# Optimization experiments

Measured on AMD Instinct MI355X. Metric: run time of the kernel, lower is better.

## Reference

```python
import jax, jax.numpy as jnp
import numpy as np

B, S, D = 2, 2048, 256
N_LAYERS, H, DK, DV, DFF = 2, 8, 32, 32, 512
EPS2 = np.float32(np.finfo(np.float32).eps) ** 2  # module uses eps*eps


def setup_inputs() -> dict:
    key = jax.random.key(0)
    ks = jax.random.split(key, 8)
    def xav(k, shape, fi, fo):
        lim = np.sqrt(6.0 / (fi + fo)).astype(np.float32)
        return jax.random.uniform(k, shape, jnp.float32, -lim, lim)
    return {
        'x': jax.random.normal(ks[0], (B, S, D), jnp.float32),
        'Wq': xav(ks[1], (N_LAYERS, H, D, DK), D, DK),
        'Wk': xav(ks[2], (N_LAYERS, H, D, DK), D, DK),
        'Wv': xav(ks[3], (N_LAYERS, H, D, DV), D, DV),
        'Wo': xav(ks[4], (N_LAYERS, H * DV, D), H * DV, D),
        'W1': xav(ks[5], (N_LAYERS, D, DFF), D, DFF),
        'b1': jnp.zeros((N_LAYERS, DFF), jnp.float32),
        'W2': xav(ks[6], (N_LAYERS, DFF, D), DFF, D),
        'b2': jnp.zeros((N_LAYERS, D), jnp.float32),
        'gamma': jnp.ones((2 * N_LAYERS,), jnp.float32),
        'beta': jnp.zeros((2 * N_LAYERS,), jnp.float32),
    }


def _layernorm(x, g, b):
    m = jnp.mean(x, axis=-1, keepdims=True)
    v = jnp.mean((x - m) ** 2, axis=-1, keepdims=True)
    return (x - m) / jnp.sqrt(v + EPS2) * g + b


def reference(x, Wq, Wk, Wv, Wo, W1, b1, W2, b2, gamma, beta):
    # mask=None in the original -> all-ones mask, a mathematical no-op.
    # NOTE: no 1/sqrt(dk) scaling, matching the source.
    n_layers = Wq.shape[0]
    for i in range(n_layers):
        q = jnp.einsum('bsd,hdk->bhsk', x, Wq[i])
        k = jnp.einsum('bsd,hdk->bhsk', x, Wk[i])
        v = jnp.einsum('bsd,hdk->bhsk', x, Wv[i])
        A = jax.nn.softmax(jnp.einsum('bhqk,bhsk->bhqs', q, k), axis=-1)
        o = jnp.einsum('bhqs,bhsk->bhqk', A, v)  # [B,h,S,dv]
        b_, h_, s_, dv_ = o.shape
        conc = o.transpose(0, 2, 1, 3).reshape(b_, s_, h_ * dv_)  # concat heads in order
        x = x + conc @ Wo[i]
        x = _layernorm(x, gamma[2 * i], beta[2 * i])
        ffn = jax.nn.relu(x @ W1[i] + b1[i]) @ W2[i] + b2[i]
        x = _layernorm(x + ffn, gamma[2 * i + 1], beta[2 * i + 1])
    return x
```

## Files before the change

### kernel.cpp

```cpp
#include <hip/hip_runtime.h>
#include <math.h>

#define BB 2
#define SS 2048
#define DD 256
#define HH 8
#define DKK 32
#define DVV 32
#define DFF 512
#define NL 2

#define KT 64
#define KSTR 40
#define VSTR 72
#define PSTR 72
#define NSPLIT 4
#define SCHUNK (SS / NSPLIT)

#define XSTR 264
#define HSTR 520
#define YSTR 260

typedef __attribute__((ext_vector_type(8))) short short8;
typedef __attribute__((ext_vector_type(4))) float f32x4;

static __device__ __forceinline__ float ln_eps2() { return 1.4210854715202004e-14f; }

static __device__ __forceinline__ ushort f2bf(float f) {
    union { float f; unsigned u; } c; c.f = f;
    unsigned r = c.u + 0x7FFFu + ((c.u >> 16) & 1u);
    return (ushort)(r >> 16);
}
static __device__ __forceinline__ float bf2f(ushort h) {
    union { unsigned u; float f; } c; c.u = ((unsigned)h) << 16;
    return c.f;
}

__global__ __launch_bounds__(256) void wtrans_kernel(
    const float* __restrict__ W1, const float* __restrict__ W2,
    ushort* __restrict__ w1t_hi, ushort* __restrict__ w1t_lo,
    ushort* __restrict__ w2t_hi, ushort* __restrict__ w2t_lo)
{
    __shared__ ushort Th[64][72];
    __shared__ ushort Tl[64][72];
    const int bid = blockIdx.x;
    const float* src; ushort *dh, *dl; int R, C, tile;
    if (bid < 64) {
        const int l = bid >> 5; tile = bid & 31;
        src = W1 + (size_t)l * DD * DFF;
        dh = w1t_hi + (size_t)l * DFF * DD; dl = w1t_lo + (size_t)l * DFF * DD;
        R = DD; C = DFF;
    } else {
        const int l = (bid - 64) >> 5; tile = (bid - 64) & 31;
        src = W2 + (size_t)l * DFF * DD;
        dh = w2t_hi + (size_t)l * DD * DFF; dl = w2t_lo + (size_t)l * DD * DFF;
        R = DFF; C = DD;
    }
    const int tilesC = C / 64;
    const int br = (tile / tilesC) * 64, bc = (tile % tilesC) * 64;
    const int tid = threadIdx.x;
#pragma unroll
    for (int i = 0; i < 16; ++i) {
        const int p = i * 256 + tid;
        const int r = p >> 6, c = p & 63;
        const float f = src[(size_t)(br + r) * C + bc + c];
        const ushort h = f2bf(f);
        Th[c][r] = h; Tl[c][r] = f2bf(f - bf2f(h));
    }
    __syncthreads();
#pragma unroll
    for (int i = 0; i < 16; ++i) {
        const int p = i * 256 + tid;
        const int r = p >> 6, c = p & 63;
        dh[(size_t)(bc + r) * R + br + c] = Th[r][c];
        dl[(size_t)(bc + r) * R + br + c] = Tl[r][c];
    }
}

__global__ __launch_bounds__(256) void wotrans_kernel(
    const float* __restrict__ Wo,
    ushort* __restrict__ wh, ushort* __restrict__ wl)
{
    __shared__ float T[64][65];
    const int l = blockIdx.x >> 4, tile = blockIdx.x & 15;
    const int tr = (tile >> 2) * 64;
    const int tc = (tile & 3) * 64;
    const float* src = Wo + (size_t)l * DD * DD;
    ushort* dh = wh + (size_t)l * DD * DD;
    ushort* dl = wl + (size_t)l * DD * DD;
    const int tid = threadIdx.x;
#pragma unroll
    for (int i = 0; i < 16; ++i) {
        const int p = i * 256 + tid;
        const int r = p >> 6, c = p & 63;
        T[r][c] = src[(size_t)(tr + r) * DD + tc + c];
    }
    __syncthreads();
#pragma unroll
    for (int i = 0; i < 16; ++i) {
        const int p = i * 256 + tid;
        const int r = p >> 6, c = p & 63;
        const float f = T[c][r];
        const size_t off = (size_t)(tc + r) * DD + tr + c;
        const ushort h = f2bf(f);
        dh[off] = h;
        dl[off] = f2bf(f - bf2f(h));
    }
}

__global__ __launch_bounds__(256) void wqkv_trans_kernel(
    const float* __restrict__ Wq, const float* __restrict__ Wk,
    const float* __restrict__ Wv,
    ushort* __restrict__ qkvT_hi, ushort* __restrict__ qkvT_lo)
{
    __shared__ float T[DKK][DD + 1];
    const int bid = blockIdx.x;
    const int l = bid / 24, rem = bid % 24, src = rem >> 3, h = rem & 7;
    const float* W = (src == 0 ? Wq : src == 1 ? Wk : Wv)
                     + ((size_t)l * HH + h) * DD * DKK;
    ushort* dh = qkvT_hi + ((size_t)l * 768 + src * 256 + h * 32) * DD;
    ushort* dl = qkvT_lo + ((size_t)l * 768 + src * 256 + h * 32) * DD;
    const int tid = threadIdx.x;
#pragma unroll
    for (int i = 0; i < 32; ++i) {
        const int p = i * 256 + tid;
        T[p & 31][p >> 5] = W[p];
    }
    __syncthreads();
#pragma unroll
    for (int i = 0; i < 32; ++i) {
        const int p = i * 256 + tid;
        const int dk = p >> 8, d = p & 255;
        const float f = T[dk][d];
        const ushort hh = f2bf(f);
        dh[dk * DD + d] = hh;
        dl[dk * DD + d] = f2bf(f - bf2f(hh));
    }
}

__global__ __launch_bounds__(256) void qkv_mfma_kernel(
    const float* __restrict__ xin,
    const ushort* __restrict__ wth, const ushort* __restrict__ wtl,
    float* __restrict__ q, ushort* __restrict__ khi, ushort* __restrict__ klo,
    ushort* __restrict__ vt)
{
    __shared__ __align__(16) ushort Xh[16 * XSTR];
    __shared__ __align__(16) ushort Xl[16 * XSTR];

    const int tid = threadIdx.x, wave = tid >> 6, lane = tid & 63;
    const int c16 = lane & 15, g = lane >> 4;
    const int row0 = (blockIdx.x >> 1) * 16;
    const int half = blockIdx.x & 1;

#pragma unroll
    for (int i = 0; i < 16; ++i) {
        const int p = i * 256 + tid;
        const int r = p >> 8, c = p & 255;
        const float f = xin[(size_t)(row0 + r) * DD + c];
        const ushort h = f2bf(f);
        Xh[r * XSTR + c] = h;
        Xl[r * XSTR + c] = f2bf(f - bf2f(h));
    }
    __syncthreads();

    short8 xf_h[8], xf_l[8];
#pragma unroll
    for (int kk = 0; kk < 8; ++kk) {
        xf_h[kk] = *(const short8*)&Xh[c16 * XSTR + kk * 32 + g * 8];
        xf_l[kk] = *(const short8*)&Xl[c16 * XSTR + kk * 32 + g * 8];
    }

    const int b = row0 / SS, s0 = row0 % SS;
    const int wbase = half * 384 + wave * 96;
#pragma unroll 2
    for (int t = 0; t < 6; ++t) {
        const int ncol = wbase + t * 16 + c16;
        const ushort* wh = wth + (size_t)ncol * DD;
        const ushort* wl = wtl + (size_t)ncol * DD;
        f32x4 acc = (f32x4)(0.f);
#pragma unroll
        for (int kk = 0; kk < 8; ++kk) {
            const short8 bh = *(const short8*)(wh + kk * 32 + g * 8);
            const short8 bl = *(const short8*)(wl + kk * 32 + g * 8);
            acc = __builtin_amdgcn_mfma_f32_16x16x32_bf16(xf_h[kk], bh, acc, 0, 0, 0);
            acc = __builtin_amdgcn_mfma_f32_16x16x32_bf16(xf_l[kk], bh, acc, 0, 0, 0);
            acc = __builtin_amdgcn_mfma_f32_16x16x32_bf16(xf_h[kk], bl, acc, 0, 0, 0);
        }
        const int src = ncol >> 8, h = (ncol >> 5) & 7, dk = ncol & 31;
        const size_t base = ((size_t)(b * HH + h) * SS + s0) * DKK + dk;
#pragma unroll
        for (int r = 0; r < 4; ++r) {
            if (src == 0) {
                q[base + (size_t)(4 * g + r) * DKK] = acc[r];
            } else if (src == 1) {
                const size_t off = base + (size_t)(4 * g + r) * DKK;
                const ushort hh = f2bf(acc[r]);
                khi[off] = hh;
                klo[off] = f2bf(acc[r] - bf2f(hh));
            } else {
                vt[((size_t)(b * HH + h) * DVV + dk) * SS + s0 + 4 * g + r] = f2bf(acc[r]);
            }
        }
    }
}

__global__ __launch_bounds__(256) void attn_mfma_kernel(
    const float* __restrict__ q, const ushort* __restrict__ khi,
    const ushort* __restrict__ klo, const ushort* __restrict__ vt,
    float* __restrict__ opart, float* __restrict__ ml)
{
    __shared__ ushort KhS[KT * KSTR];
    __shared__ ushort KlS[KT * KSTR];
    __shared__ ushort VtS[32 * VSTR];
    __shared__ ushort PlS[4 * 16 * PSTR];

    const int tid  = threadIdx.x;
    const int wave = tid >> 6;
    const int lane = tid & 63;
    const int c16  = lane & 15;
    const int g    = lane >> 4;

    const int nqb = SS / 64;
    const int bh  = blockIdx.x / (nqb * NSPLIT);
    const int rem = blockIdx.x % (nqb * NSPLIT);
    const int qb  = rem / NSPLIT;
    const int sp  = rem % NSPLIT;
    const int qbase = qb * 64 + wave * 16;

    const float*  qp  = q   + (size_t)bh * SS * DKK;
    const ushort* khp = khi + (size_t)bh * SS * DKK;
    const ushort* klp = klo + (size_t)bh * SS * DKK;
    const ushort* vtp = vt  + (size_t)bh * DVV * SS;

    short8 qhi, qlo;
    {
        const float* qr = qp + (size_t)(qbase + c16) * DKK + g * 8;
#pragma unroll
        for (int j = 0; j < 8; ++j) {
            const ushort h = f2bf(qr[j]);
            qhi[j] = (short)h;
            qlo[j] = (short)f2bf(qr[j] - bf2f(h));
        }
    }

    float m_r[4], l_r[4];
    f32x4 oacc0, oacc1;
#pragma unroll
    for (int r = 0; r < 4; ++r) { m_r[r] = -1e30f; l_r[r] = 0.f; }
    oacc0 = (f32x4)(0.f); oacc1 = (f32x4)(0.f);
    const f32x4 zero = (f32x4)(0.f);

    ushort* Pw = PlS + wave * 16 * PSTR;

    for (int kt = sp * SCHUNK; kt < (sp + 1) * SCHUNK; kt += KT) {
#pragma unroll
        for (int i = 0; i < 2; ++i) {
            const int p = i * 256 + tid;
            const int row = p >> 3;
            const int col4 = (p & 7) * 4;
            const uint2 h8 = *(const uint2*)(khp + (size_t)(kt + row) * DKK + col4);
            const uint2 l8 = *(const uint2*)(klp + (size_t)(kt + row) * DKK + col4);
            *(uint2*)&KhS[row * KSTR + col4] = h8;
            *(uint2*)&KlS[row * KSTR + col4] = l8;
        }
#pragma unroll
        for (int i = 0; i < 2; ++i) {
            const int p = i * 256 + tid;
            const int dv = p >> 4;
            const int s8 = (p & 15) * 4;
            const uint2 v8 = *(const uint2*)(vtp + (size_t)dv * SS + kt + s8);
            *(uint2*)&VtS[dv * VSTR + s8] = v8;
        }
        __syncthreads();

        f32x4 sc[4];
#pragma unroll
        for (int t = 0; t < 4; ++t) {
            const short8 khf = *(const short8*)&KhS[(t * 16 + c16) * KSTR + g * 8];
            const short8 klf = *(const short8*)&KlS[(t * 16 + c16) * KSTR + g * 8];
            f32x4 s = __builtin_amdgcn_mfma_f32_16x16x32_bf16(qlo, khf, zero, 0, 0, 0);
            s = __builtin_amdgcn_mfma_f32_16x16x32_bf16(qhi, klf, s, 0, 0, 0);
            s = __builtin_amdgcn_mfma_f32_16x16x32_bf16(qhi, khf, s, 0, 0, 0);
            sc[t] = s;
        }

#pragma unroll
        for (int r = 0; r < 4; ++r) {
            float tm = sc[0][r];
#pragma unroll
            for (int t = 1; t < 4; ++t) tm = fmaxf(tm, sc[t][r]);
            tm = fmaxf(tm, __shfl_xor(tm, 1));
            tm = fmaxf(tm, __shfl_xor(tm, 2));
            tm = fmaxf(tm, __shfl_xor(tm, 4));
            tm = fmaxf(tm, __shfl_xor(tm, 8));
            const float nm = fmaxf(m_r[r], tm);
            const float scale = __expf(m_r[r] - nm);
            m_r[r] = nm;
            float psum = 0.f;
#pragma unroll
            for (int t = 0; t < 4; ++t) {
                const float p = __expf(sc[t][r] - nm);
                sc[t][r] = p;
                psum += p;
            }
            psum += __shfl_xor(psum, 1);
            psum += __shfl_xor(psum, 2);
            psum += __shfl_xor(psum, 4);
            psum += __shfl_xor(psum, 8);
            l_r[r] = l_r[r] * scale + psum;
            oacc0[r] *= scale;
            oacc1[r] *= scale;
        }

#pragma unroll
        for (int t = 0; t < 4; ++t)
#pragma unroll
            for (int r = 0; r < 4; ++r)
                Pw[(g * 4 + r) * PSTR + t * 16 + c16] = f2bf(sc[t][r]);

#pragma unroll
        for (int s4 = 0; s4 < 2; ++s4) {
            const short8 pfrag  = *(const short8*)&Pw[c16 * PSTR + s4 * 32 + g * 8];
            const short8 vfrag0 = *(const short8*)&VtS[c16 * VSTR + s4 * 32 + g * 8];
            const short8 vfrag1 = *(const short8*)&VtS[(16 + c16) * VSTR + s4 * 32 + g * 8];
            oacc0 = __builtin_amdgcn_mfma_f32_16x16x32_bf16(pfrag, vfrag0, oacc0, 0, 0, 0);
            oacc1 = __builtin_amdgcn_mfma_f32_16x16x32_bf16(pfrag, vfrag1, oacc1, 0, 0, 0);
        }
        __syncthreads();
    }

    const size_t pbase = (size_t)(sp * BB * HH + bh) * SS;
#pragma unroll
    for (int r = 0; r < 4; ++r) {
        const int qrow = qbase + g * 4 + r;
        float* op = opart + (pbase + qrow) * DVV;
        op[c16]      = oacc0[r];
        op[16 + c16] = oacc1[r];
        if (c16 == 0) {
            ml[(pbase + qrow) * 2]     = m_r[r];
            ml[(pbase + qrow) * 2 + 1] = l_r[r];
        }
    }
}

__global__ __launch_bounds__(256) void attn_merge_kernel(
    const float* __restrict__ opart, const float* __restrict__ ml,
    float* __restrict__ o)
{
    const int nch = SS / 128;
    const int bh = blockIdx.x / nch;
    const int chunk = blockIdx.x % nch;
    const int q0 = chunk * 128;
    const int b = bh >> 3, h = bh & 7;
    const int tid = threadIdx.x;

#pragma unroll
    for (int i = 0; i < 16; ++i) {
        const int p = i * 256 + tid;
        const int ql = p >> 5, dv = p & 31;
        const int qr = q0 + ql;
        float ms[NSPLIT], ls[NSPLIT];
#pragma unroll
        for (int s = 0; s < NSPLIT; ++s) {
            const size_t pb = (size_t)(s * BB * HH + bh) * SS + qr;
            ms[s] = ml[pb * 2];
            ls[s] = ml[pb * 2 + 1];
        }
        float M = ms[0];
#pragma unroll
        for (int s = 1; s < NSPLIT; ++s) M = fmaxf(M, ms[s]);
        float L = 0.f, acc = 0.f;
#pragma unroll
        for (int s = 0; s < NSPLIT; ++s) {
            const float w = __expf(ms[s] - M);
            L += w * ls[s];
            acc += w * opart[((size_t)(s * BB * HH + bh) * SS + qr) * DVV + dv];
        }
        o[(size_t)(b * SS + qr) * (HH * DVV) + h * DVV + dv] = acc / L;
    }
}

__global__ __launch_bounds__(256) void proj_mfma_kernel(
    const float* __restrict__ conc, const float* __restrict__ xres,
    const ushort* __restrict__ wth, const ushort* __restrict__ wtl,
    const float* __restrict__ gamma, const float* __restrict__ beta,
    float* __restrict__ xout)
{
    __shared__ __align__(16) ushort Xh[16 * XSTR];
    __shared__ __align__(16) ushort Xl[16 * XSTR];
    __shared__ float Y[16 * YSTR];

    const int tid = threadIdx.x, wave = tid >> 6, lane = tid & 63;
    const int c16 = lane & 15, g = lane >> 4;
    const int row0 = blockIdx.x * 16;

#pragma unroll
    for (int i = 0; i < 16; ++i) {
        const int p = i * 256 + tid;
        const int r = p >> 8, c = p & 255;
        const float f = conc[(size_t)(row0 + r) * DD + c];
        const ushort h = f2bf(f);
        Xh[r * XSTR + c] = h;
        Xl[r * XSTR + c] = f2bf(f - bf2f(h));
    }
    __syncthreads();

    short8 xf_h[8], xf_l[8];
#pragma unroll
    for (int kk = 0; kk < 8; ++kk) {
        xf_h[kk] = *(const short8*)&Xh[c16 * XSTR + kk * 32 + g * 8];
        xf_l[kk] = *(const short8*)&Xl[c16 * XSTR + kk * 32 + g * 8];
    }

    const int wbase = wave * 64;
#pragma unroll 2
    for (int t = 0; t < 4; ++t) {
        const int ncol = wbase + t * 16 + c16;
        const ushort* wh = wth + (size_t)ncol * DD;
        const ushort* wl = wtl + (size_t)ncol * DD;
        f32x4 acc = (f32x4)(0.f);
#pragma unroll
        for (int kk = 0; kk < 8; ++kk) {
            const short8 bh = *(const short8*)(wh + kk * 32 + g * 8);
            const short8 bl = *(const short8*)(wl + kk * 32 + g * 8);
            acc = __builtin_amdgcn_mfma_f32_16x16x32_bf16(xf_h[kk], bh, acc, 0, 0, 0);
            acc = __builtin_amdgcn_mfma_f32_16x16x32_bf16(xf_l[kk], bh, acc, 0, 0, 0);
            acc = __builtin_amdgcn_mfma_f32_16x16x32_bf16(xf_h[kk], bl, acc, 0, 0, 0);
        }
#pragma unroll
        for (int r = 0; r < 4; ++r)
            Y[(4 * g + r) * YSTR + ncol] = acc[r];
    }
    __syncthreads();

    const float g0 = gamma[0], b0 = beta[0];
#pragma unroll
    for (int rr = 0; rr < 4; ++rr) {
        const int row = wave * 4 + rr;
        float v[4];
        float sum = 0.f;
#pragma unroll
        for (int j = 0; j < 4; ++j) {
            const int c = lane + 64 * j;
            v[j] = Y[row * YSTR + c] + xres[(size_t)(row0 + row) * DD + c];
            sum += v[j];
        }
#pragma unroll
        for (int m = 32; m >= 1; m >>= 1) sum += __shfl_xor(sum, m);
        const float mean = sum * (1.0f / DD);
        float var = 0.f;
#pragma unroll
        for (int j = 0; j < 4; ++j) { v[j] -= mean; var += v[j] * v[j]; }
#pragma unroll
        for (int m = 32; m >= 1; m >>= 1) var += __shfl_xor(var, m);
        var *= (1.0f / DD);
        const float rstd = 1.0f / sqrtf(var + ln_eps2());
#pragma unroll
        for (int j = 0; j < 4; ++j)
            xout[(size_t)(row0 + row) * DD + lane + 64 * j] = v[j] * rstd * g0 + b0;
    }
}

__global__ __launch_bounds__(256) void ffn_mfma_kernel(
    const float* __restrict__ xin,
    const ushort* __restrict__ w1th, const ushort* __restrict__ w1tl,
    const ushort* __restrict__ w2th, const ushort* __restrict__ w2tl,
    const float* __restrict__ b1, const float* __restrict__ b2,
    const float* __restrict__ gamma, const float* __restrict__ beta,
    float* __restrict__ xout)
{
    __shared__ __align__(16) char smem[(2 * 16 * XSTR + 2 * 16 * HSTR) * 2];
    ushort* Xh = (ushort*)smem;
    ushort* Xl = Xh + 16 * XSTR;
    ushort* Hh = Xl + 16 * XSTR;
    ushort* Hl = Hh + 16 * HSTR;
    float*  Y  = (float*)smem;

    const int tid  = threadIdx.x;
    const int wave = tid >> 6;
    const int lane = tid & 63;
    const int c16  = lane & 15;
    const int g    = lane >> 4;
    const int row0 = blockIdx.x * 16;

#pragma unroll
    for (int i = 0; i < 16; ++i) {
        const int p = i * 256 + tid;
        const int r = p >> 8, c = p & 255;
        const float f = xin[(size_t)(row0 + r) * DD + c];
        const ushort h = f2bf(f);
        Xh[r * XSTR + c] = h;
        Xl[r * XSTR + c] = f2bf(f - bf2f(h));
    }
    __syncthreads();

    short8 xf_h[8], xf_l[8];
#pragma unroll
    for (int kk = 0; kk < 8; ++kk) {
        xf_h[kk] = *(const short8*)&Xh[c16 * XSTR + kk * 32 + g * 8];
        xf_l[kk] = *(const short8*)&Xl[c16 * XSTR + kk * 32 + g * 8];
    }

    const int wbase = wave * 128;
#pragma unroll 2
    for (int t = 0; t < 8; ++t) {
        const int ncol = wbase + t * 16 + c16;
        const ushort* wh = w1th + (size_t)ncol * DD;
        const ushort* wl = w1tl + (size_t)ncol * DD;
        f32x4 acc = (f32x4)(0.f);
#pragma unroll
        for (int kk = 0; kk < 8; ++kk) {
            const short8 bh = *(const short8*)(wh + kk * 32 + g * 8);
            const short8 bl = *(const short8*)(wl + kk * 32 + g * 8);
            acc = __builtin_amdgcn_mfma_f32_16x16x32_bf16(xf_h[kk], bh, acc, 0, 0, 0);
            acc = __builtin_amdgcn_mfma_f32_16x16x32_bf16(xf_l[kk], bh, acc, 0, 0, 0);
            acc = __builtin_amdgcn_mfma_f32_16x16x32_bf16(xf_h[kk], bl, acc, 0, 0, 0);
        }
        const float bias = b1[ncol];
#pragma unroll
        for (int r = 0; r < 4; ++r) {
            const int m = 4 * g + r;
            const float hv = fmaxf(acc[r] + bias, 0.f);
            const ushort hh = f2bf(hv);
            Hh[m * HSTR + ncol] = hh;
            Hl[m * HSTR + ncol] = f2bf(hv - bf2f(hh));
        }
    }
    __syncthreads();

    const int obase = wave * 64;
    f32x4 acc2[4];
#pragma unroll
    for (int t = 0; t < 4; ++t) acc2[t] = (f32x4)(0.f);
#pragma unroll 2
    for (int kk = 0; kk < 16; ++kk) {
        const short8 ah = *(const short8*)&Hh[c16 * HSTR + kk * 32 + g * 8];
        const short8 al = *(const short8*)&Hl[c16 * HSTR + kk * 32 + g * 8];
#pragma unroll
        for (int t = 0; t < 4; ++t) {
            const int ncol = obase + t * 16 + c16;
            const short8 bh = *(const short8*)(w2th + (size_t)ncol * DFF + kk * 32 + g * 8);
            const short8 bl = *(const short8*)(w2tl + (size_t)ncol * DFF + kk * 32 + g * 8);
            acc2[t] = __builtin_amdgcn_mfma_f32_16x16x32_bf16(ah, bh, acc2[t], 0, 0, 0);
            acc2[t] = __builtin_amdgcn_mfma_f32_16x16x32_bf16(al, bh, acc2[t], 0, 0, 0);
            acc2[t] = __builtin_amdgcn_mfma_f32_16x16x32_bf16(ah, bl, acc2[t], 0, 0, 0);
        }
    }

#pragma unroll
    for (int t = 0; t < 4; ++t) {
        const int ncol = obase + t * 16 + c16;
#pragma unroll
        for (int r = 0; r < 4; ++r)
            Y[(4 * g + r) * YSTR + ncol] = acc2[t][r];
    }
    __syncthreads();

    const float g0 = gamma[0], b0 = beta[0];
#pragma unroll
    for (int rr = 0; rr < 4; ++rr) {
        const int row = wave * 4 + rr;
        float v[4];
        float sum = 0.f;
#pragma unroll
        for (int j = 0; j < 4; ++j) {
            const int c = lane + 64 * j;
            v[j] = Y[row * YSTR + c] + b2[c] + xin[(size_t)(row0 + row) * DD + c];
            sum += v[j];
        }
#pragma unroll
        for (int m = 32; m >= 1; m >>= 1) sum += __shfl_xor(sum, m);
        const float mean = sum * (1.0f / DD);
        float var = 0.f;
#pragma unroll
        for (int j = 0; j < 4; ++j) { v[j] -= mean; var += v[j] * v[j]; }
#pragma unroll
        for (int m = 32; m >= 1; m >>= 1) var += __shfl_xor(var, m);
        var *= (1.0f / DD);
        const float rstd = 1.0f / sqrtf(var + ln_eps2());
#pragma unroll
        for (int j = 0; j < 4; ++j)
            xout[(size_t)(row0 + row) * DD + lane + 64 * j] = v[j] * rstd * g0 + b0;
    }
}

extern "C" void kernel_launch(void* const* d_in, const int* in_sizes, int n_in,
                              void* d_out, int out_size, void* d_ws, size_t ws_size,
                              hipStream_t stream) {
    const float* x     = (const float*)d_in[0];
    const float* Wq    = (const float*)d_in[1];
    const float* Wk    = (const float*)d_in[2];
    const float* Wv    = (const float*)d_in[3];
    const float* Wo    = (const float*)d_in[4];
    const float* W1    = (const float*)d_in[5];
    const float* b1    = (const float*)d_in[6];
    const float* W2    = (const float*)d_in[7];
    const float* b2    = (const float*)d_in[8];
    const float* gamma = (const float*)d_in[9];
    const float* beta  = (const float*)d_in[10];
    float* out = (float*)d_out;

    const size_t NTOK = (size_t)BB * SS * DD;
    const size_t WFF  = (size_t)NL * DFF * DD;
    const size_t WOO  = (size_t)NL * DD * DD;
    const size_t WQKV = (size_t)NL * 768 * DD;
    float*  q    = (float*)d_ws;
    ushort* khi  = (ushort*)(q + NTOK);
    ushort* klo  = khi + NTOK;
    ushort* vt   = klo + NTOK;
    float*  o    = (float*)(vt + NTOK);
    float*  xa   = o + NTOK;
    float*  xb   = xa + NTOK;
    ushort* w1th = (ushort*)(xb + NTOK);
    ushort* w1tl = w1th + WFF;
    ushort* w2th = w1tl + WFF;
    ushort* w2tl = w2th + WFF;
    ushort* woth = w2tl + WFF;
    ushort* wotl = woth + WOO;
    ushort* wqth = wotl + WOO;
    ushort* wqtl = wqth + WQKV;
    float*  opart = (float*)(wqtl + WQKV);
    float*  ml    = opart + (size_t)NSPLIT * BB * HH * SS * DVV;

    wtrans_kernel<<<128, 256, 0, stream>>>(W1, W2, w1th, w1tl, w2th, w2tl);
    wotrans_kernel<<<NL * 16, 256, 0, stream>>>(Wo, woth, wotl);
    wqkv_trans_kernel<<<48, 256, 0, stream>>>(Wq, Wk, Wv, wqth, wqtl);

    const float* cur = x;
    for (int l = 0; l < NL; ++l) {
        qkv_mfma_kernel<<<2 * BB * SS / 16, 256, 0, stream>>>(
            cur, wqth + (size_t)l * 768 * DD, wqtl + (size_t)l * 768 * DD,
            q, khi, klo, vt);
        attn_mfma_kernel<<<BB * HH * (SS / 64) * NSPLIT, 256, 0, stream>>>(
            q, khi, klo, vt, opart, ml);
        attn_merge_kernel<<<BB * HH * (SS / 128), 256, 0, stream>>>(opart, ml, o);
        proj_mfma_kernel<<<BB * SS / 16, 256, 0, stream>>>(
            o, cur, woth + (size_t)l * DD * DD, wotl + (size_t)l * DD * DD,
            gamma + 2 * l, beta + 2 * l, xa);
        float* nxt = (l == NL - 1) ? out : xb;
        ffn_mfma_kernel<<<BB * SS / 16, 256, 0, stream>>>(
            xa, w1th + (size_t)l * DFF * DD, w1tl + (size_t)l * DFF * DD,
            w2th + (size_t)l * DD * DFF, w2tl + (size_t)l * DD * DFF,
            b1 + (size_t)l * DFF, b2 + (size_t)l * DD,
            gamma + 2 * l + 1, beta + 2 * l + 1, nxt);
        cur = nxt;
    }
}
```

Baseline: 299.3 us.

## Rewrite attention with 32x32 MFMA and transposed scores kept in registers

The attention kernel now uses 32x32x16 bf16 MFMA with each wave owning 32 query rows, and computes S^T = K·Q so each lane holds a full query column. The row max and sum then need only one cross-half shuffle instead of four-step reductions. P is packed to bf16 with v_cvt_pk_bf16_f32 and rearranged through lane shuffles rather than a round trip through LDS, and the block covers 128 queries, halving the grid. The risks are more register pressure from the 16-wide accumulators, fewer blocks to fill the CUs, and a changed bf16 rounding path for P.

```diff
diff --git a/kernel.cpp b/kernel.cpp
--- a/kernel.cpp
+++ b/kernel.cpp
@@ -10,10 +10,8 @@
 #define DFF 512
 #define NL 2
 
-#define KT 64
 #define KSTR 40
 #define VSTR 72
-#define PSTR 72
 #define NSPLIT 4
 #define SCHUNK (SS / NSPLIT)
 
@@ -23,6 +21,7 @@
 
 typedef __attribute__((ext_vector_type(8))) short short8;
 typedef __attribute__((ext_vector_type(4))) float f32x4;
+typedef __attribute__((ext_vector_type(16))) float f32x16;
 
 static __device__ __forceinline__ float ln_eps2() { return 1.4210854715202004e-14f; }
 
@@ -34,6 +33,11 @@
 static __device__ __forceinline__ float bf2f(ushort h) {
     union { unsigned u; float f; } c; c.u = ((unsigned)h) << 16;
     return c.f;
+}
+static __device__ __forceinline__ unsigned cvtpk_bf16(float a, float b) {
+    unsigned r;
+    asm volatile("v_cvt_pk_bf16_f32 %0, %1, %2" : "=v"(r) : "v"(a), "v"(b));
+    return r;
 }
 
 __global__ __launch_bounds__(256) void wtrans_kernel(
@@ -209,50 +213,49 @@
     const ushort* __restrict__ klo, const ushort* __restrict__ vt,
     float* __restrict__ opart, float* __restrict__ ml)
 {
-    __shared__ ushort KhS[KT * KSTR];
-    __shared__ ushort KlS[KT * KSTR];
+    __shared__ ushort KhS[64 * KSTR];
+    __shared__ ushort KlS[64 * KSTR];
     __shared__ ushort VtS[32 * VSTR];
-    __shared__ ushort PlS[4 * 16 * PSTR];
 
     const int tid  = threadIdx.x;
     const int wave = tid >> 6;
     const int lane = tid & 63;
-    const int c16  = lane & 15;
-    const int g    = lane >> 4;
-
-    const int nqb = SS / 64;
+    const int c32  = lane & 31;
+    const int hi   = lane >> 5;
+
+    const int nqb = SS / 128;
     const int bh  = blockIdx.x / (nqb * NSPLIT);
     const int rem = blockIdx.x % (nqb * NSPLIT);
     const int qb  = rem / NSPLIT;
     const int sp  = rem % NSPLIT;
-    const int qbase = qb * 64 + wave * 16;
+    const int qrow = qb * 128 + wave * 32 + c32;
 
     const float*  qp  = q   + (size_t)bh * SS * DKK;
     const ushort* khp = khi + (size_t)bh * SS * DKK;
     const ushort* klp = klo + (size_t)bh * SS * DKK;
     const ushort* vtp = vt  + (size_t)bh * DVV * SS;
 
-    short8 qhi, qlo;
+    short8 qh0, ql0, qh1, ql1;
     {
-        const float* qr = qp + (size_t)(qbase + c16) * DKK + g * 8;
+        const float* qr = qp + (size_t)qrow * DKK + hi * 8;
 #pragma unroll
         for (int j = 0; j < 8; ++j) {
             const ushort h = f2bf(qr[j]);
-            qhi[j] = (short)h;
-            qlo[j] = (short)f2bf(qr[j] - bf2f(h));
-        }
-    }
-
-    float m_r[4], l_r[4];
-    f32x4 oacc0, oacc1;
-#pragma unroll
-    for (int r = 0; r < 4; ++r) { m_r[r] = -1e30f; l_r[r] = 0.f; }
-    oacc0 = (f32x4)(0.f); oacc1 = (f32x4)(0.f);
-    const f32x4 zero = (f32x4)(0.f);
-
-    ushort* Pw = PlS + wave * 16 * PSTR;
-
-    for (int kt = sp * SCHUNK; kt < (sp + 1) * SCHUNK; kt += KT) {
+            qh0[j] = (short)h; ql0[j] = (short)f2bf(qr[j] - bf2f(h));
+        }
+#pragma unroll
+        for (int j = 0; j < 8; ++j) {
+            const float f = qr[16 + j];
+            const ushort h = f2bf(f);
+            qh1[j] = (short)h; ql1[j] = (short)f2bf(f - bf2f(h));
+        }
+    }
+
+    float m = -1e30f, l = 0.f;
+    f32x16 oacc = (f32x16)(0.f);
+    const f32x16 zero16 = (f32x16)(0.f);
+
+    for (int kt = sp * SCHUNK; kt < (sp + 1) * SCHUNK; kt += 64) {
 #pragma unroll
         for (int i = 0; i < 2; ++i) {
             const int p = i * 256 + tid;
@@ -273,73 +276,118 @@
         }
         __syncthreads();
 
-        f32x4 sc[4];
-#pragma unroll
-        for (int t = 0; t < 4; ++t) {
-            const short8 khf = *(const short8*)&KhS[(t * 16 + c16) * KSTR + g * 8];
-            const short8 klf = *(const short8*)&KlS[(t * 16 + c16) * KSTR + g * 8];
-            f32x4 s = __builtin_amdgcn_mfma_f32_16x16x32_bf16(qlo, khf, zero, 0, 0, 0);
-            s = __builtin_amdgcn_mfma_f32_16x16x32_bf16(qhi, klf, s, 0, 0, 0);
-            s = __builtin_amdgcn_mfma_f32_16x16x32_bf16(qhi, khf, s, 0, 0, 0);
-            sc[t] = s;
-        }
-
-#pragma unroll
-        for (int r = 0; r < 4; ++r) {
-            float tm = sc[0][r];
-#pragma unroll
-            for (int t = 1; t < 4; ++t) tm = fmaxf(tm, sc[t][r]);
-            tm = fmaxf(tm, __shfl_xor(tm, 1));
-            tm = fmaxf(tm, __shfl_xor(tm, 2));
-            tm = fmaxf(tm, __shfl_xor(tm, 4));
-            tm = fmaxf(tm, __shfl_xor(tm, 8));
-            const float nm = fmaxf(m_r[r], tm);
-            const float scale = __expf(m_r[r] - nm);
-            m_r[r] = nm;
-            float psum = 0.f;
-#pragma unroll
-            for (int t = 0; t < 4; ++t) {
-                const float p = __expf(sc[t][r] - nm);
-                sc[t][r] = p;
-                psum += p;
-            }
-            psum += __shfl_xor(psum, 1);
-            psum += __shfl_xor(psum, 2);
-            psum += __shfl_xor(psum, 4);
-            psum += __shfl_xor(psum, 8);
-            l_r[r] = l_r[r] * scale + psum;
-            oacc0[r] *= scale;
-            oacc1[r] *= scale;
-        }
-
-#pragma unroll
-        for (int t = 0; t < 4; ++t)
-#pragma unroll
-            for (int r = 0; r < 4; ++r)
-                Pw[(g * 4 + r) * PSTR + t * 16 + c16] = f2bf(sc[t][r]);
-
-#pragma unroll
-        for (int s4 = 0; s4 < 2; ++s4) {
-            const short8 pfrag  = *(const short8*)&Pw[c16 * PSTR + s4 * 32 + g * 8];
-            const short8 vfrag0 = *(const short8*)&VtS[c16 * VSTR + s4 * 32 + g * 8];
-            const short8 vfrag1 = *(const short8*)&VtS[(16 + c16) * VSTR + s4 * 32 + g * 8];
-            oacc0 = __builtin_amdgcn_mfma_f32_16x16x32_bf16(pfrag, vfrag0, oacc0, 0, 0, 0);
-            oacc1 = __builtin_amdgcn_mfma_f32_16x16x32_bf16(pfrag, vfrag1, oacc1, 0, 0, 0);
+        f32x16 s0, s1;
+        {
+            const int rb0 = c32 * KSTR + hi * 8;
+            const short8 kh0 = *(const short8*)&KhS[rb0];
+            const short8 kl0 = *(const short8*)&KlS[rb0];
+            const short8 kh1 = *(const short8*)&KhS[rb0 + 16];
+            const short8 kl1 = *(const short8*)&KlS[rb0 + 16];
+            f32x16 s = __builtin_amdgcn_mfma_f32_32x32x16_bf16(kh0, ql0, zero16, 0, 0, 0);
+            s = __builtin_amdgcn_mfma_f32_32x32x16_bf16(kl0, qh0, s, 0, 0, 0);
+            s = __builtin_amdgcn_mfma_f32_32x32x16_bf16(kh0, qh0, s, 0, 0, 0);
+            s = __builtin_amdgcn_mfma_f32_32x32x16_bf16(kh1, ql1, s, 0, 0, 0);
+            s = __builtin_amdgcn_mfma_f32_32x32x16_bf16(kl1, qh1, s, 0, 0, 0);
+            s0 = __builtin_amdgcn_mfma_f32_32x32x16_bf16(kh1, qh1, s, 0, 0, 0);
+        }
+        {
+            const int rb1 = (32 + c32) * KSTR + hi * 8;
+            const short8 kh0 = *(const short8*)&KhS[rb1];
+            const short8 kl0 = *(const short8*)&KlS[rb1];
+            const short8 kh1 = *(const short8*)&KhS[rb1 + 16];
+            const short8 kl1 = *(const short8*)&KlS[rb1 + 16];
+            f32x16 s = __builtin_amdgcn_mfma_f32_32x32x16_bf16(kh0, ql0, zero16, 0, 0, 0);
+            s = __builtin_amdgcn_mfma_f32_32x32x16_bf16(kl0, qh0, s, 0, 0, 0);
+            s = __builtin_amdgcn_mfma_f32_32x32x16_bf16(kh0, qh0, s, 0, 0, 0);
+            s = __builtin_amdgcn_mfma_f32_32x32x16_bf16(kh1, ql1, s, 0, 0, 0);
+            s = __builtin_amdgcn_mfma_f32_32x32x16_bf16(kl1, qh1, s, 0, 0, 0);
+            s1 = __builtin_amdgcn_mfma_f32_32x32x16_bf16(kh1, qh1, s, 0, 0, 0);
+        }
+
+        float tm = s0[0];
+#pragma unroll
+        for (int j = 1; j < 16; ++j) tm = fmaxf(tm, s0[j]);
+#pragma unroll
+        for (int j = 0; j < 16; ++j) tm = fmaxf(tm, s1[j]);
+        tm = fmaxf(tm, __shfl_xor(tm, 32));
+        const float nm = fmaxf(m, tm);
+        const float scale = __expf(m - nm);
+        m = nm;
+        float psum = 0.f;
+#pragma unroll
+        for (int j = 0; j < 16; ++j) { const float p = __expf(s0[j] - nm); s0[j] = p; psum += p; }
+#pragma unroll
+        for (int j = 0; j < 16; ++j) { const float p = __expf(s1[j] - nm); s1[j] = p; psum += p; }
+        psum += __shfl_xor(psum, 32);
+        l = l * scale + psum;
+#pragma unroll
+        for (int j = 0; j < 16; ++j) oacc[j] *= scale;
+
+        unsigned w0 = cvtpk_bf16(s0[0],  s0[1]);
+        unsigned w1 = cvtpk_bf16(s0[2],  s0[3]);
+        unsigned w2 = cvtpk_bf16(s0[4],  s0[5]);
+        unsigned w3 = cvtpk_bf16(s0[6],  s0[7]);
+        unsigned w4 = cvtpk_bf16(s0[8],  s0[9]);
+        unsigned w5 = cvtpk_bf16(s0[10], s0[11]);
+        unsigned w6 = cvtpk_bf16(s0[12], s0[13]);
+        unsigned w7 = cvtpk_bf16(s0[14], s0[15]);
+        unsigned u0 = cvtpk_bf16(s1[0],  s1[1]);
+        unsigned u1 = cvtpk_bf16(s1[2],  s1[3]);
+        unsigned u2 = cvtpk_bf16(s1[4],  s1[5]);
+        unsigned u3 = cvtpk_bf16(s1[6],  s1[7]);
+        unsigned u4 = cvtpk_bf16(s1[8],  s1[9]);
+        unsigned u5 = cvtpk_bf16(s1[10], s1[11]);
+        unsigned u6 = cvtpk_bf16(s1[12], s1[13]);
+        unsigned u7 = cvtpk_bf16(s1[14], s1[15]);
+
+        const unsigned x0 = __shfl_xor(hi ? w0 : w2, 32);
+        const unsigned x1 = __shfl_xor(hi ? w1 : w3, 32);
+        const unsigned x2 = __shfl_xor(hi ? w4 : w6, 32);
+        const unsigned x3 = __shfl_xor(hi ? w5 : w7, 32);
+        const unsigned y0 = __shfl_xor(hi ? u0 : u2, 32);
+        const unsigned y1 = __shfl_xor(hi ? u1 : u3, 32);
+        const unsigned y2 = __shfl_xor(hi ? u4 : u6, 32);
+        const unsigned y3 = __shfl_xor(hi ? u5 : u7, 32);
+
+        union { unsigned u[4]; short8 s8; } pa, pb, pc, pd;
+        if (hi == 0) {
+            pa.u[0] = w0; pa.u[1] = w1; pa.u[2] = x0; pa.u[3] = x1;
+            pb.u[0] = w4; pb.u[1] = w5; pb.u[2] = x2; pb.u[3] = x3;
+            pc.u[0] = u0; pc.u[1] = u1; pc.u[2] = y0; pc.u[3] = y1;
+            pd.u[0] = u4; pd.u[1] = u5; pd.u[2] = y2; pd.u[3] = y3;
+        } else {
+            pa.u[0] = x0; pa.u[1] = x1; pa.u[2] = w2; pa.u[3] = w3;
+            pb.u[0] = x2; pb.u[1] = x3; pb.u[2] = w6; pb.u[3] = w7;
+            pc.u[0] = y0; pc.u[1] = y1; pc.u[2] = u2; pc.u[3] = u3;
+            pd.u[0] = y2; pd.u[1] = y3; pd.u[2] = u6; pd.u[3] = u7;
+        }
+
+        {
+            const int vb = c32 * VSTR + hi * 8;
+            const short8 v0 = *(const short8*)&VtS[vb];
+            const short8 v1 = *(const short8*)&VtS[vb + 16];
+            const short8 v2 = *(const short8*)&VtS[vb + 32];
+            const short8 v3 = *(const short8*)&VtS[vb + 48];
+            oacc = __builtin_amdgcn_mfma_f32_32x32x16_bf16(v0, pa.s8, oacc, 0, 0, 0);
+            oacc = __builtin_amdgcn_mfma_f32_32x32x16_bf16(v1, pb.s8, oacc, 0, 0, 0);
+            oacc = __builtin_amdgcn_mfma_f32_32x32x16_bf16(v2, pc.s8, oacc, 0, 0, 0);
+            oacc = __builtin_amdgcn_mfma_f32_32x32x16_bf16(v3, pd.s8, oacc, 0, 0, 0);
         }
         __syncthreads();
     }
 
     const size_t pbase = (size_t)(sp * BB * HH + bh) * SS;
-#pragma unroll
-    for (int r = 0; r < 4; ++r) {
-        const int qrow = qbase + g * 4 + r;
-        float* op = opart + (pbase + qrow) * DVV;
-        op[c16]      = oacc0[r];
-        op[16 + c16] = oacc1[r];
-        if (c16 == 0) {
-            ml[(pbase + qrow) * 2]     = m_r[r];
-            ml[(pbase + qrow) * 2 + 1] = l_r[r];
-        }
+    float* op = opart + (pbase + qrow) * DVV;
+#pragma unroll
+    for (int q4 = 0; q4 < 4; ++q4) {
+        f32x4 v;
+        v[0] = oacc[4 * q4 + 0]; v[1] = oacc[4 * q4 + 1];
+        v[2] = oacc[4 * q4 + 2]; v[3] = oacc[4 * q4 + 3];
+        *(f32x4*)(op + 8 * q4 + 4 * hi) = v;
+    }
+    if (hi == 0) {
+        ml[(pbase + qrow) * 2]     = m;
+        ml[(pbase + qrow) * 2 + 1] = l;
     }
 }
 
@@ -519,11 +567,11 @@
         const float bias = b1[ncol];
 #pragma unroll
         for (int r = 0; r < 4; ++r) {
-            const int m = 4 * g + r;
+            const int mm = 4 * g + r;
             const float hv = fmaxf(acc[r] + bias, 0.f);
             const ushort hh = f2bf(hv);
-            Hh[m * HSTR + ncol] = hh;
-            Hl[m * HSTR + ncol] = f2bf(hv - bf2f(hh));
+            Hh[mm * HSTR + ncol] = hh;
+            Hl[mm * HSTR + ncol] = f2bf(hv - bf2f(hh));
         }
     }
     __syncthreads();
@@ -631,7 +679,7 @@
         qkv_mfma_kernel<<<2 * BB * SS / 16, 256, 0, stream>>>(
             cur, wqth + (size_t)l * 768 * DD, wqtl + (size_t)l * 768 * DD,
             q, khi, klo, vt);
-        attn_mfma_kernel<<<BB * HH * (SS / 64) * NSPLIT, 256, 0, stream>>>(
+        attn_mfma_kernel<<<BB * HH * (SS / 128) * NSPLIT, 256, 0, stream>>>(
             q, khi, klo, vt, opart, ml);
         attn_merge_kernel<<<BB * HH * (SS / 128), 256, 0, stream>>>(opart, ml, o);
         proj_mfma_kernel<<<BB * SS / 16, 256, 0, stream>>>(
```

Result: faster. 244.6 us (median of 3 runs) (-18.3%).
